# Kernel optimization log

Hardware: AMD Instinct MI355X
Metric: run time of the kernel (lower is better)

Reference implementation:

```python
import jax, jax.numpy as jnp
import numpy as np

LEAKY_SLOPE = 0.25
EPS_COS = 1e-8
EPS_NORM = 1e-12


def cosine_dist(x):
    # 1 - cosine similarity, matching cosine_distance_torch
    w = jnp.linalg.norm(x, axis=1, keepdims=True)  # [n,1]
    return 1.0 - (x @ x.T) / jnp.maximum(w * w.T, EPS_COS)


def gen_adj(x, edge_per_node):
    # gen_tr_adj_mat: threshold = (edge_per_node*n)-th smallest pairwise cosine distance,
    # zero diagonal, symmetrize via elementwise max, add I, L1 row-normalize.
    n = x.shape[0]
    dist = cosine_dist(x)  # [n,n]
    k = edge_per_node * n
    param = jax.lax.stop_gradient(jnp.partition(dist.ravel(), k)[k])
    eye = jnp.eye(n, dtype=x.dtype)
    g = (dist <= param).astype(x.dtype) * (1.0 - eye)
    adj = (1.0 - dist) * g
    adj_t = adj.T
    take_t = (adj_t > adj).astype(x.dtype)
    adj = adj + adj_t * take_t - adj * take_t  # elementwise max-symmetrize
    adj = adj + eye
    row_norm = jnp.maximum(jnp.sum(jnp.abs(adj), axis=1, keepdims=True), EPS_NORM)
    return adj / row_norm


def gcn_layer(x, adj, w, b):
    # dense mm -> (sparse) adj mm -> bias -> leaky_relu
    return jax.nn.leaky_relu(adj @ (x @ w) + b, LEAKY_SLOPE)


def setup_inputs() -> dict:
    key = jax.random.key(0)
    ks = jax.random.split(key, 8)
    n, d = 4000, 1000
    h = [400, 400, 200]
    x = jax.random.normal(ks[0], (n, d), jnp.float32)

    def xavier(k, fi, fo):
        std = (2.0 / (fi + fo)) ** 0.5
        return std * jax.random.normal(k, (fi, fo), jnp.float32)

    w1 = xavier(ks[1], d, h[0])
    w2 = xavier(ks[2], h[0], h[1])
    w3 = xavier(ks[3], h[1], h[2])
    b1 = jnp.zeros((h[0],), jnp.float32)
    b2 = jnp.zeros((h[1],), jnp.float32)
    b3 = jnp.zeros((h[2],), jnp.float32)
    adj_parameter = 10
    adj = gen_adj(x, adj_parameter)  # initial train adjacency, as in the pipeline
    return dict(adj_parameter=adj_parameter, x=x, adj=adj,
                w1=w1, b1=b1, w2=w2, b2=b2, w3=w3, b3=b3)


def reference(adj_parameter, x, adj, w1, b1, w2, b2, w3, b3):
    # eval mode: F.dropout(training=False) is identity
    x = gcn_layer(x, adj, w1, b1)
    adj = gen_adj(x, adj_parameter)
    x = gcn_layer(x, adj, w2, b2)
    adj = gen_adj(x, adj_parameter)
    x = gcn_layer(x, adj, w3, b3)
    return x
```

## Files before the change

### kernel.cpp

```cpp
#include <hip/hip_runtime.h>
#include <math.h>

#define NN 4000
#define KC 384
#define LEAKY 0.25f
#define HBLK 1000
#define NPART1 2016


template<int EPI>
__device__ inline float epi_apply(float v, int r, int c,
                                  const float* __restrict__ bias,
                                  const float* __restrict__ wn)
{
    if (EPI == 1) {
        float s = __fadd_rn(v, bias[c]);
        return (s >= 0.f) ? s : __fmul_rn(LEAKY, s);
    }
    if (EPI == 2) {
        float den = fmaxf(__fmul_rn(wn[r], wn[c]), 1e-8f);
        return __fsub_rn(1.0f, __fdiv_rn(v, den));
    }
    return v;
}

template<int XF>
__device__ float xf(float v)
{
    if (XF == 0) return __fmul_rn(v, v);
    return fabsf(v);
}

template<int XF>
__device__ float np_pairwise(const float* a, int n)
{
    if (n < 8) {
        float r = 0.f;
        for (int i = 0; i < n; ++i) r = __fadd_rn(r, xf<XF>(a[i]));
        return r;
    }
    if (n <= 128) {
        float r[8];
#pragma unroll
        for (int j = 0; j < 8; ++j) r[j] = xf<XF>(a[j]);
        int i = 8;
        const int lim = n - (n & 7);
        for (; i < lim; i += 8)
#pragma unroll
            for (int j = 0; j < 8; ++j) r[j] = __fadd_rn(r[j], xf<XF>(a[i + j]));
        float res = __fadd_rn(__fadd_rn(__fadd_rn(r[0], r[1]), __fadd_rn(r[2], r[3])),
                              __fadd_rn(__fadd_rn(r[4], r[5]), __fadd_rn(r[6], r[7])));
        for (; i < n; ++i) res = __fadd_rn(res, xf<XF>(a[i]));
        return res;
    }
    int n2 = (n / 2) & ~7;
    return __fadd_rn(np_pairwise<XF>(a, n2), np_pairwise<XF>(a + n2, n - n2));
}

__global__ __launch_bounds__(256, 4)
void gemm_tri64_k(const float* __restrict__ A, float* __restrict__ C,
                  unsigned* __restrict__ partial, int n, int K,
                  const float* __restrict__ wn)
{
    __shared__ float As[16][68];
    __shared__ float Bs[16][68];
    __shared__ unsigned lh[2048];
    const int tid = threadIdx.x;
    const int tx = tid & 15, ty = tid >> 4;
    const int sub = tid & 7;
    const int nt = (n + 63) >> 6;
    int bi = 0, rem = blockIdx.x;
    while (rem >= nt - bi) { rem -= nt - bi; ++bi; }
    const int bm = bi * 64, bn = (bi + rem) * 64;
    const bool diag = (rem == 0);

    for (int i = tid; i < 2048; i += 256) lh[i] = 0;

    float blk[4][4] = {};
    float acc[4][4];
    bool first = true;

    for (int kb = 0; kb < K; kb += KC) {
        const int kend = (kb + KC < K) ? kb + KC : K;
        for (int k0 = kb; k0 < kend; k0 += 16) {
            {
                int row = tid >> 2, q = tid & 3;
                int gr = bm + row, gk = k0 + q * 4;
                float4 v = make_float4(0.f, 0.f, 0.f, 0.f);
                if (gr < n) {
                    if (gk + 3 < kend) {
                        v = *(const float4*)(A + (size_t)gr * K + gk);
                    } else {
                        float* vp = (float*)&v;
#pragma unroll
                        for (int e = 0; e < 4; ++e)
                            if (gk + e < kend) vp[e] = A[(size_t)gr * K + gk + e];
                    }
                }
                float* vp = (float*)&v;
#pragma unroll
                for (int e = 0; e < 4; ++e) As[q * 4 + e][row] = vp[e];
            }
            {
                int row = tid >> 2, q = tid & 3;
                int gc = bn + row, gk = k0 + q * 4;
                float4 v = make_float4(0.f, 0.f, 0.f, 0.f);
                if (gc < n) {
                    if (gk + 3 < kend) {
                        v = *(const float4*)(A + (size_t)gc * K + gk);
                    } else {
                        float* vp = (float*)&v;
#pragma unroll
                        for (int e = 0; e < 4; ++e)
                            if (gk + e < kend) vp[e] = A[(size_t)gc * K + gk + e];
                    }
                }
                float* vp = (float*)&v;
#pragma unroll
                for (int e = 0; e < 4; ++e) Bs[q * 4 + e][row] = vp[e];
            }
            __syncthreads();
#pragma unroll
            for (int kk = 0; kk < 16; ++kk) {
                float a[4], b[4];
                *(float4*)&a[0] = *(const float4*)&As[kk][ty * 4];
                *(float4*)&b[0] = *(const float4*)&Bs[kk][tx * 4];
#pragma unroll
                for (int i = 0; i < 4; ++i)
#pragma unroll
                    for (int j = 0; j < 4; ++j)
                        blk[i][j] = fmaf(a[i], b[j], blk[i][j]);
            }
            __syncthreads();
        }
        if (first) {
#pragma unroll
            for (int i = 0; i < 4; ++i)
#pragma unroll
                for (int j = 0; j < 4; ++j) { acc[i][j] = blk[i][j]; blk[i][j] = 0.f; }
            first = false;
        } else {
#pragma unroll
            for (int i = 0; i < 4; ++i)
#pragma unroll
                for (int j = 0; j < 4; ++j) {
                    acc[i][j] = __fadd_rn(acc[i][j], blk[i][j]);
                    blk[i][j] = 0.f;
                }
        }
    }

#pragma unroll
    for (int i = 0; i < 4; ++i) {
        int r = bm + ty * 4 + i;
        if (r >= n) continue;
        float* Crow = C + (size_t)r * n;
        int c = bn + tx * 4;
        float v[4];
#pragma unroll
        for (int e = 0; e < 4; ++e)
            v[e] = epi_apply<2>(acc[i][e], r, c + e, nullptr, wn);
        if (c + 3 < n) {
            float4 s; s.x = v[0]; s.y = v[1]; s.z = v[2]; s.w = v[3];
            *(float4*)(Crow + c) = s;
        } else {
#pragma unroll
            for (int e = 0; e < 4; ++e)
                if (c + e < n) Crow[c + e] = v[e];
        }
#pragma unroll
        for (int e = 0; e < 4; ++e) {
            int cc = c + e;
            if (cc >= n) continue;
            unsigned w = 2u;
            if (diag) {
                if (cc < r) continue;
                if (cc == r) w = 1u;
            }
            unsigned u = __float_as_uint(v[e]);
            unsigned key = (u & 0x80000000u) ? ~u : (u | 0x80000000u);
            atomicAdd(&lh[(((key >> 24) & 0xFFu) << 3) | sub], w);
        }
    }
    __syncthreads();
    unsigned t = 0;
#pragma unroll
    for (int s = 0; s < 8; ++s) t += lh[(tid << 3) | s];
    partial[blockIdx.x * 256 + tid] = t;
}

template<int EPI>
__global__ __launch_bounds__(256, 4)
void gemm_s_k(const float* __restrict__ A, const float* __restrict__ B,
              float* __restrict__ C, int M, int N, int K,
              const float* __restrict__ bias)
{
    __shared__ float As[16][68];
    __shared__ float Bs[16][68];
    const int tid = threadIdx.x;
    const int tx = tid & 15, ty = tid >> 4;
    const int bm = blockIdx.y * 64, bn = blockIdx.x * 64;

    float blk[4][4] = {};
    float acc[4][4];
    bool first = true;

    for (int kb = 0; kb < K; kb += KC) {
        const int kend = (kb + KC < K) ? kb + KC : K;
        for (int k0 = kb; k0 < kend; k0 += 16) {
            {
                int row = tid >> 2, q = tid & 3;
                int gr = bm + row, gk = k0 + q * 4;
                float4 v = make_float4(0.f, 0.f, 0.f, 0.f);
                if (gr < M) {
                    if (gk + 3 < kend) {
                        v = *(const float4*)(A + (size_t)gr * K + gk);
                    } else {
                        float* vp = (float*)&v;
#pragma unroll
                        for (int e = 0; e < 4; ++e)
                            if (gk + e < kend) vp[e] = A[(size_t)gr * K + gk + e];
                    }
                }
                float* vp = (float*)&v;
#pragma unroll
                for (int e = 0; e < 4; ++e) As[q * 4 + e][row] = vp[e];
            }
            {
                int kk = tid >> 4, c = (tid & 15) * 4;
                int gk = k0 + kk, gc = bn + c;
                float4 v = make_float4(0.f, 0.f, 0.f, 0.f);
                if (gk < kend) {
                    if (gc + 3 < N) {
                        v = *(const float4*)(B + (size_t)gk * N + gc);
                    } else {
                        float* vp = (float*)&v;
#pragma unroll
                        for (int e = 0; e < 4; ++e)
                            if (gc + e < N) vp[e] = B[(size_t)gk * N + gc + e];
                    }
                }
                *(float4*)&Bs[kk][c] = v;
            }
            __syncthreads();
#pragma unroll
            for (int kk = 0; kk < 16; ++kk) {
                float a[4], b[4];
                *(float4*)&a[0] = *(const float4*)&As[kk][ty * 4];
                *(float4*)&b[0] = *(const float4*)&Bs[kk][tx * 4];
#pragma unroll
                for (int i = 0; i < 4; ++i)
#pragma unroll
                    for (int j = 0; j < 4; ++j)
                        blk[i][j] = fmaf(a[i], b[j], blk[i][j]);
            }
            __syncthreads();
        }
        if (first) {
#pragma unroll
            for (int i = 0; i < 4; ++i)
#pragma unroll
                for (int j = 0; j < 4; ++j) { acc[i][j] = blk[i][j]; blk[i][j] = 0.f; }
            first = false;
        } else {
#pragma unroll
            for (int i = 0; i < 4; ++i)
#pragma unroll
                for (int j = 0; j < 4; ++j) {
                    acc[i][j] = __fadd_rn(acc[i][j], blk[i][j]);
                    blk[i][j] = 0.f;
                }
        }
    }

#pragma unroll
    for (int i = 0; i < 4; ++i) {
        int r = bm + ty * 4 + i;
        if (r >= M) continue;
        float* Crow = C + (size_t)r * N;
        int c = bn + tx * 4;
        float v[4];
#pragma unroll
        for (int e = 0; e < 4; ++e)
            v[e] = epi_apply<EPI>(acc[i][e], r, c + e, bias, nullptr);
        if (c + 3 < N) {
            float4 s; s.x = v[0]; s.y = v[1]; s.z = v[2]; s.w = v[3];
            *(float4*)(Crow + c) = s;
        } else {
#pragma unroll
            for (int e = 0; e < 4; ++e)
                if (c + e < N) Crow[c + e] = v[e];
        }
    }
}

template<int EPI, bool TRANSB, bool FIRST, bool LAST>
__global__ __launch_bounds__(256, 4)
void gemm_pass_k(const float* __restrict__ A, const float* __restrict__ B,
                 float* __restrict__ C, int M, int N, int K, int kb, int kend,
                 const float* __restrict__ bias, const float* __restrict__ wn)
{
    __shared__ float As[16][132];
    __shared__ float Bs[16][132];
    const int tid = threadIdx.x;
    const int tx = tid & 15, ty = tid >> 4;
    const int bm = blockIdx.y * 128, bn = blockIdx.x * 128;

    float blk[8][8] = {};

    for (int k0 = kb; k0 < kend; k0 += 16) {
#pragma unroll
        for (int it = 0; it < 2; ++it) {
            int idx = tid + it * 256;
            int row = idx >> 2, q = idx & 3;
            int gr = bm + row, gk = k0 + q * 4;
            float4 v = make_float4(0.f, 0.f, 0.f, 0.f);
            if (gr < M) {
                if (gk + 3 < kend) {
                    v = *(const float4*)(A + (size_t)gr * K + gk);
                } else {
                    float* vp = (float*)&v;
#pragma unroll
                    for (int e = 0; e < 4; ++e)
                        if (gk + e < kend) vp[e] = A[(size_t)gr * K + gk + e];
                }
            }
            float* vp = (float*)&v;
#pragma unroll
            for (int e = 0; e < 4; ++e) As[q * 4 + e][row] = vp[e];
        }
        if (!TRANSB) {
#pragma unroll
            for (int it = 0; it < 2; ++it) {
                int idx = tid + it * 256;
                int kk = idx >> 5, cq = idx & 31;
                int gk = k0 + kk, c = cq * 4, gc = bn + c;
                float4 v = make_float4(0.f, 0.f, 0.f, 0.f);
                if (gk < kend) {
                    if (gc + 3 < N) {
                        v = *(const float4*)(B + (size_t)gk * N + gc);
                    } else {
                        float* vp = (float*)&v;
#pragma unroll
                        for (int e = 0; e < 4; ++e)
                            if (gc + e < N) vp[e] = B[(size_t)gk * N + gc + e];
                    }
                }
                *(float4*)&Bs[kk][c] = v;
            }
        } else {
#pragma unroll
            for (int it = 0; it < 2; ++it) {
                int idx = tid + it * 256;
                int row = idx >> 2, q = idx & 3;
                int gc = bn + row, gk = k0 + q * 4;
                float4 v = make_float4(0.f, 0.f, 0.f, 0.f);
                if (gc < N) {
                    if (gk + 3 < kend) {
                        v = *(const float4*)(B + (size_t)gc * K + gk);
                    } else {
                        float* vp = (float*)&v;
#pragma unroll
                        for (int e = 0; e < 4; ++e)
                            if (gk + e < kend) vp[e] = B[(size_t)gc * K + gk + e];
                    }
                }
                float* vp = (float*)&v;
#pragma unroll
                for (int e = 0; e < 4; ++e) Bs[q * 4 + e][row] = vp[e];
            }
        }
        __syncthreads();
#pragma unroll
        for (int kk = 0; kk < 16; ++kk) {
            float a[8], b[8];
            *(float4*)&a[0] = *(const float4*)&As[kk][ty * 4];
            *(float4*)&a[4] = *(const float4*)&As[kk][ty * 4 + 64];
            *(float4*)&b[0] = *(const float4*)&Bs[kk][tx * 4];
            *(float4*)&b[4] = *(const float4*)&Bs[kk][tx * 4 + 64];
#pragma unroll
            for (int i = 0; i < 8; ++i)
#pragma unroll
                for (int j = 0; j < 8; ++j)
                    blk[i][j] = fmaf(a[i], b[j], blk[i][j]);
        }
        __syncthreads();
    }

#pragma unroll
    for (int i = 0; i < 8; ++i) {
        int r = bm + ty * 4 + (i & 3) + (i >> 2) * 64;
        if (r >= M) continue;
        float* Crow = C + (size_t)r * N;
#pragma unroll
        for (int h = 0; h < 2; ++h) {
            int c = bn + tx * 4 + h * 64;
            float v[4];
#pragma unroll
            for (int e = 0; e < 4; ++e) v[e] = blk[i][h * 4 + e];
            if (c + 3 < N) {
                if (!FIRST) {
                    float4 o = *(const float4*)(Crow + c);
                    v[0] = __fadd_rn(o.x, v[0]); v[1] = __fadd_rn(o.y, v[1]);
                    v[2] = __fadd_rn(o.z, v[2]); v[3] = __fadd_rn(o.w, v[3]);
                }
                if (LAST) {
#pragma unroll
                    for (int e = 0; e < 4; ++e)
                        v[e] = epi_apply<EPI>(v[e], r, c + e, bias, wn);
                }
                float4 s; s.x = v[0]; s.y = v[1]; s.z = v[2]; s.w = v[3];
                *(float4*)(Crow + c) = s;
            } else {
#pragma unroll
                for (int e = 0; e < 4; ++e) {
                    if (c + e >= N) continue;
                    float vv = v[e];
                    if (!FIRST) vv = __fadd_rn(Crow[c + e], vv);
                    if (LAST) vv = epi_apply<EPI>(vv, r, c + e, bias, wn);
                    Crow[c + e] = vv;
                }
            }
        }
    }
}

__global__ __launch_bounds__(256)
void rownorm2_k(const float* __restrict__ X, float* __restrict__ wn)
{
    __shared__ float buf[400];
    __shared__ float leaf[4];
    const int row = blockIdx.x;
    const float* Xr = X + (size_t)row * 400;
    for (int i = threadIdx.x; i < 100; i += 256)
        *(float4*)&buf[i * 4] = *(const float4*)(Xr + i * 4);
    __syncthreads();
    if (threadIdx.x < 4) {
        const int off = (threadIdx.x >> 1) * 200 + ((threadIdx.x & 1) ? 96 : 0);
        const int len = (threadIdx.x & 1) ? 104 : 96;
        leaf[threadIdx.x] = np_pairwise<0>(buf + off, len);
    }
    __syncthreads();
    if (threadIdx.x == 0) {
        float s = __fadd_rn(__fadd_rn(leaf[0], leaf[1]),
                            __fadd_rn(leaf[2], leaf[3]));
        wn[row] = __fsqrt_rn(s);
    }
}

__global__ __launch_bounds__(256)
void rowabs2_k(const float* __restrict__ A, float* __restrict__ rs)
{
    __shared__ float buf[4000];
    __shared__ float leaf[8];
    const int row = blockIdx.x;
    const float* Ar = A + (size_t)row * 4000;
    for (int i = threadIdx.x; i < 1000; i += 256)
        *(float4*)&buf[i * 4] = *(const float4*)(Ar + i * 4);
    __syncthreads();
    if (threadIdx.x < 8) {
        const int off = (threadIdx.x >> 1) * 1000 + ((threadIdx.x & 1) ? 496 : 0);
        const int len = (threadIdx.x & 1) ? 504 : 496;
        leaf[threadIdx.x] = np_pairwise<1>(buf + off, len);
    }
    __syncthreads();
    if (threadIdx.x == 0) {
        float s = __fadd_rn(
            __fadd_rn(__fadd_rn(leaf[0], leaf[1]), __fadd_rn(leaf[2], leaf[3])),
            __fadd_rn(__fadd_rn(leaf[4], leaf[5]), __fadd_rn(leaf[6], leaf[7])));
        rs[row] = fmaxf(s, 1e-12f);
    }
}

__global__ void init_k(unsigned* __restrict__ state, const void* __restrict__ epn,
                       int* __restrict__ cnt)
{
    const int t = blockIdx.x * 256 + threadIdx.x;
    if (t < NN) cnt[t] = 0;
    if (t == 0) {
        int k = ((const int*)epn)[0];
        if (k <= 0 || k > 4000) {
            float f = ((const float*)epn)[0];
            if (f > 0.f && f <= 4000.f) k = (int)f;
            else {
                long long ll = ((const long long*)epn)[0];
                if (ll > 0 && ll <= 4000) k = (int)ll;
                else {
                    double dd = ((const double*)epn)[0];
                    k = (dd > 0.0 && dd <= 4000.0) ? (int)dd : 10;
                }
            }
        }
        state[0] = 0u;
        state[1] = (unsigned)(k * NN);
    }
}

__global__ __launch_bounds__(256)
void hist_tri_k(const float* __restrict__ dist, unsigned* __restrict__ partial,
                const unsigned* __restrict__ state, int shift, int n)
{
    __shared__ unsigned lh[2048];
    for (int i = threadIdx.x; i < 2048; i += 256) lh[i] = 0;
    __syncthreads();
    const unsigned prefix = state[0];
    const int sub = threadIdx.x & 7;
    const int npair = (n + 1) / 2;
    for (int p = blockIdx.x; p < npair; p += HBLK) {
#pragma unroll
        for (int half = 0; half < 2; ++half) {
            const int i = half ? (n - 1 - p) : p;
            if (half && i == p) break;
            const float* row = dist + (size_t)i * n;
            for (int j = i + threadIdx.x; j < n; j += 256) {
                unsigned u = __float_as_uint(row[j]);
                unsigned key = (u & 0x80000000u) ? ~u : (u | 0x80000000u);
                bool ok = ((key >> (shift + 8)) == prefix);
                if (ok) atomicAdd(&lh[((((key >> shift) & 0xFFu)) << 3) | sub],
                                  (j == i) ? 1u : 2u);
            }
        }
    }
    __syncthreads();
    unsigned t = 0;
#pragma unroll
    for (int s = 0; s < 8; ++s) t += lh[(threadIdx.x << 3) | s];
    partial[blockIdx.x * 256 + threadIdx.x] = t;
}

__global__ __launch_bounds__(256)
void reduce_k(const unsigned* __restrict__ partial, int nparts,
              unsigned* __restrict__ hist256)
{
    const int bin = blockIdx.x;
    const int tid = threadIdx.x;
    unsigned s = 0;
    for (int i = tid; i < nparts; i += 256)
        s += partial[(size_t)i * 256 + bin];
    __shared__ unsigned sh[256];
    sh[tid] = s;
    __syncthreads();
    for (int off = 128; off > 0; off >>= 1) {
        if (tid < off) sh[tid] += sh[tid + off];
        __syncthreads();
    }
    if (tid == 0) hist256[bin] = sh[0];
}

__global__ __launch_bounds__(256)
void scan256_k(const unsigned* __restrict__ hist256, unsigned* __restrict__ state,
               int shift, float* __restrict__ param)
{
    const int tid = threadIdx.x;
    unsigned h = hist256[tid];
    __shared__ unsigned sh[256];
    sh[tid] = h;
    __syncthreads();
    for (int off = 1; off < 256; off <<= 1) {
        unsigned v = (tid >= off) ? sh[tid - off] : 0;
        __syncthreads();
        sh[tid] += v;
        __syncthreads();
    }
    const unsigned incl = sh[tid], excl = incl - h;
    const unsigned krem = state[1];
    if (krem >= excl && krem < incl) {
        unsigned np = (state[0] << 8) | (unsigned)tid;
        state[0] = np;
        state[1] = krem - excl;
        if (shift == 0) {
            unsigned u = (np & 0x80000000u) ? (np ^ 0x80000000u) : ~np;
            *param = __uint_as_float(u);
        }
    }
}

__device__ inline float thr_f(float d, int i, int j, float p)
{
    float a = (d <= p && i != j) ? __fsub_rn(1.0f, d) : 0.0f;
    return (i == j) ? 1.0f : a;
}

__global__ __launch_bounds__(256)
void symthresh_mirror_k(float* __restrict__ adj, const float* __restrict__ param,
                        int* __restrict__ cnt, int n)
{
    __shared__ float TB[64][65];
    const float p = *param;
    const int nt = (n + 63) >> 6;
    int bi = 0, rem = blockIdx.x;
    while (rem >= nt - bi) { rem -= nt - bi; ++bi; }
    const int bj = bi + rem;
    const int tid = threadIdx.x;
    const int lane = tid & 63;
    const int r0i = bi * 64, r0j = bj * 64;

#pragma unroll
    for (int it = 0; it < 16; ++it) {
        int idx = tid + it * 256;
        int q = idx >> 6, c = idx & 63;
        int gr = r0i + q, gc = r0j + c;
        bool inb = (gr < n && gc < n);
        float a = 0.f;
        if (inb) {
            a = thr_f(adj[(size_t)gr * n + gc], gr, gc, p);
            adj[(size_t)gr * n + gc] = a;
            TB[q][c] = a;
        }
        unsigned long long m = __ballot(inb && a != 0.0f);
        if (lane == 0 && gr < n) atomicAdd(&cnt[gr], (int)__popcll(m));
    }
    __syncthreads();
    if (bi != bj) {
#pragma unroll
        for (int it = 0; it < 16; ++it) {
            int idx = tid + it * 256;
            int q = idx >> 6, c = idx & 63;
            int gr = r0j + q, gc = r0i + c;
            bool inb = (gr < n && gc < n);
            float a = 0.f;
            if (inb) {
                a = TB[c][q];
                adj[(size_t)gr * n + gc] = a;
            }
            unsigned long long m = __ballot(inb && a != 0.0f);
            if (lane == 0 && gr < n) atomicAdd(&cnt[gr], (int)__popcll(m));
        }
    }
}

__global__ __launch_bounds__(256)
void norm_k(float* __restrict__ adj, const float* __restrict__ rs, int n)
{
    const int i = blockIdx.y;
    const int j = blockIdx.x * 256 + threadIdx.x;
    if (j >= n) return;
    const size_t idx = (size_t)i * n + j;
    adj[idx] = __fdiv_rn(adj[idx], rs[i]);
}

__global__ __launch_bounds__(256)
void count_k(const float* __restrict__ A, int* __restrict__ cnt, int n)
{
    const int gw = (blockIdx.x * blockDim.x + threadIdx.x) >> 6;
    if (gw >= n) return;
    const int lane = threadIdx.x & 63;
    int c = 0;
    for (int k0 = 0; k0 < n; k0 += 64) {
        int k = k0 + lane;
        bool nz = (k < n) && (A[(size_t)gw * n + k] != 0.0f);
        unsigned long long m = __ballot(nz);
        c += (int)__popcll(m);
    }
    if (lane == 0) cnt[gw] = c;
}

__global__ __launch_bounds__(1024)
void scanrows_k(const int* __restrict__ cnt, int* __restrict__ roff)
{
    const int t = threadIdx.x;
    int vals[4];
    int s0 = 0;
#pragma unroll
    for (int e = 0; e < 4; ++e) {
        int r = t * 4 + e;
        vals[e] = (r < NN) ? cnt[r] : 0;
        s0 += vals[e];
    }
    __shared__ int sh[1024];
    sh[t] = s0;
    __syncthreads();
    for (int off = 1; off < 1024; off <<= 1) {
        int v = (t >= off) ? sh[t - off] : 0;
        __syncthreads();
        sh[t] += v;
        __syncthreads();
    }
    int excl = sh[t] - s0;
#pragma unroll
    for (int e = 0; e < 4; ++e) {
        int r = t * 4 + e;
        if (r <= NN) roff[r] = excl;
        excl += vals[e];
    }
    if (t == 1023) roff[NN] = sh[1023];
}

template<bool DIV>
__global__ __launch_bounds__(256)
void fill_k(const float* __restrict__ A, const int* __restrict__ roff,
            const float* __restrict__ rs, int* __restrict__ ridx,
            float* __restrict__ rval, int n)
{
    const int gw = (blockIdx.x * blockDim.x + threadIdx.x) >> 6;
    if (gw >= n) return;
    const int lane = threadIdx.x & 63;
    const float r = DIV ? rs[gw] : 1.0f;
    int base = roff[gw];
    const unsigned long long ltmask = (lane == 63) ? ~0ULL >> 1
                                                   : ((1ULL << lane) - 1);
    for (int k0 = 0; k0 < n; k0 += 64) {
        int k = k0 + lane;
        float v = (k < n) ? A[(size_t)gw * n + k] : 0.f;
        bool nz = (v != 0.0f);
        unsigned long long m = __ballot(nz);
        if (nz) {
            int pos = base + (int)__popcll(m & ltmask);
            ridx[pos] = k;
            rval[pos] = DIV ? __fdiv_rn(v, r) : v;
        }
        base += (int)__popcll(m);
    }
}

template<bool WN>
__global__ __launch_bounds__(256)
void spmm_k(const int* __restrict__ roff, const int* __restrict__ ridx,
            const float* __restrict__ rval, const float* __restrict__ T,
            const float* __restrict__ bias, float* __restrict__ H, int ncols,
            float* __restrict__ wn)
{
    __shared__ int ks[128];
    __shared__ float vs[128];
    __shared__ float buf[512];
    __shared__ float leaf[4];
    const int r = blockIdx.x;
    const int tid = threadIdx.x;
    const int c0 = tid, c1 = tid + 256;
    const bool ok0 = c0 < ncols, ok1 = c1 < ncols;
    float acc0 = 0.f, blk0 = 0.f, acc1 = 0.f, blk1 = 0.f;
    int nb = KC;
    const int s = roff[r], e = roff[r + 1];
    for (int base = s; base < e; base += 128) {
        const int m = (e - base < 128) ? (e - base) : 128;
        __syncthreads();
        if (tid < m) { ks[tid] = ridx[base + tid]; vs[tid] = rval[base + tid]; }
        __syncthreads();
        for (int t = 0; t < m; ++t) {
            const int k = ks[t];
            const float v = vs[t];
            while (k >= nb) {
                acc0 = __fadd_rn(acc0, blk0); blk0 = 0.f;
                acc1 = __fadd_rn(acc1, blk1); blk1 = 0.f;
                nb += KC;
            }
            const float* Tr = T + (size_t)k * ncols;
            if (ok0) blk0 = fmaf(v, Tr[c0], blk0);
            if (ok1) blk1 = fmaf(v, Tr[c1], blk1);
        }
    }
    acc0 = __fadd_rn(acc0, blk0);
    acc1 = __fadd_rn(acc1, blk1);
    float h0 = 0.f, h1 = 0.f;
    if (ok0) {
        float s0 = __fadd_rn(acc0, bias[c0]);
        h0 = (s0 >= 0.f) ? s0 : __fmul_rn(LEAKY, s0);
        H[(size_t)r * ncols + c0] = h0;
    }
    if (ok1) {
        float s1 = __fadd_rn(acc1, bias[c1]);
        h1 = (s1 >= 0.f) ? s1 : __fmul_rn(LEAKY, s1);
        H[(size_t)r * ncols + c1] = h1;
    }
    if (WN) {
        if (ok0) buf[c0] = h0;
        if (ok1) buf[c1] = h1;
        __syncthreads();
        if (tid < 4) {
            const int off = (tid >> 1) * 200 + ((tid & 1) ? 96 : 0);
            const int len = (tid & 1) ? 104 : 96;
            leaf[tid] = np_pairwise<0>(buf + off, len);
        }
        __syncthreads();
        if (tid == 0) {
            float s2 = __fadd_rn(__fadd_rn(leaf[0], leaf[1]),
                                 __fadd_rn(leaf[2], leaf[3]));
            wn[r] = __fsqrt_rn(s2);
        }
    }
}

template<int EPI, bool TRANSB>
static void run_gemm(const float* A, const float* B, float* C,
                     int M, int N, int K, const float* bias, const float* wn,
                     hipStream_t stream)
{
    const int nb = (K + KC - 1) / KC;
    const dim3 grid((N + 127) / 128, (M + 127) / 128);
    for (int p = 0; p < nb; ++p) {
        const int kb = p * KC;
        const int kend = (kb + KC < K) ? kb + KC : K;
        const bool first = (p == 0), last = (p == nb - 1);
        if (first && last)
            gemm_pass_k<EPI, TRANSB, true, true><<<grid, 256, 0, stream>>>(
                A, B, C, M, N, K, kb, kend, bias, wn);
        else if (first)
            gemm_pass_k<EPI, TRANSB, true, false><<<grid, 256, 0, stream>>>(
                A, B, C, M, N, K, kb, kend, bias, wn);
        else if (last)
            gemm_pass_k<EPI, TRANSB, false, true><<<grid, 256, 0, stream>>>(
                A, B, C, M, N, K, kb, kend, bias, wn);
        else
            gemm_pass_k<EPI, TRANSB, false, false><<<grid, 256, 0, stream>>>(
                A, B, C, M, N, K, kb, kend, bias, wn);
    }
}

extern "C" void kernel_launch(void* const* d_in, const int* in_sizes, int n_in,
                              void* d_out, int out_size, void* d_ws, size_t ws_size,
                              hipStream_t stream)
{
    const void*  epn  = d_in[0];
    const float* x    = (const float*)d_in[1];
    const float* adj0 = (const float*)d_in[2];
    const float* w1   = (const float*)d_in[3];
    const float* b1   = (const float*)d_in[4];
    const float* w2   = (const float*)d_in[5];
    const float* b2   = (const float*)d_in[6];
    const float* w3   = (const float*)d_in[7];
    const float* b3   = (const float*)d_in[8];
    float* out = (float*)d_out;

    char* ws = (char*)d_ws;
    float*    dist    = (float*)   ws;
    float*    Tbuf    = (float*)  (ws + 64000000);
    float*    H1      = (float*)  (ws + 70400000);
    float*    H2      = (float*)  (ws + 76800000);
    float*    wn      = (float*)  (ws + 83200000);
    float*    rs      = (float*)  (ws + 83216000);
    unsigned* state   = (unsigned*)(ws + 83232000);
    float*    param   = (float*)  (ws + 83232008);
    unsigned* hist256 = (unsigned*)(ws + 83232064);
    unsigned* partial = (unsigned*)(ws + 83233088);
    int*      cnt     = (int*)    (ws + 85297472);
    int*      roff    = (int*)    (ws + 85313472);
    int*      ridx    = (int*)    (ws + 85329480);
    float*    rval    = (float*)  (ws + 101329480);
    const bool use_csr = (ws_size >= 117329480ULL + 64);

    const int gsN = (NN + 63) / 64;
    const int nt64 = (NN + 63) / 64;
    const int nsym64 = nt64 * (nt64 + 1) / 2;

    auto genadj = [&](const float* H, bool have_wn) {
        if (!have_wn)
            rownorm2_k<<<NN, 256, 0, stream>>>(H, wn);
        gemm_tri64_k<<<nsym64, 256, 0, stream>>>(H, dist, partial, NN, 400, wn);
        init_k<<<16, 256, 0, stream>>>(state, epn, cnt);
        reduce_k<<<256, 256, 0, stream>>>(partial, NPART1, hist256);
        scan256_k<<<1, 256, 0, stream>>>(hist256, state, 24, param);
        for (int p = 1; p < 4; ++p) {
            const int shift = 24 - 8 * p;
            hist_tri_k<<<HBLK, 256, 0, stream>>>(dist, partial, state, shift, NN);
            reduce_k<<<256, 256, 0, stream>>>(partial, HBLK, hist256);
            scan256_k<<<1, 256, 0, stream>>>(hist256, state, shift, param);
        }
        symthresh_mirror_k<<<nsym64, 256, 0, stream>>>(dist, param, cnt, NN);
        rowabs2_k<<<NN, 256, 0, stream>>>(dist, rs);
    };

    auto aggregate_pre = [&](const float* Aadj, const float* Tm,
                             const float* bias, float* Hout, int ncols,
                             bool want_wn) {
        if (use_csr) {
            count_k<<<(NN + 3) / 4, 256, 0, stream>>>(Aadj, cnt, NN);
            scanrows_k<<<1, 1024, 0, stream>>>(cnt, roff);
            fill_k<false><<<(NN + 3) / 4, 256, 0, stream>>>(Aadj, roff, nullptr,
                                                            ridx, rval, NN);
            if (want_wn)
                spmm_k<true><<<NN, 256, 0, stream>>>(roff, ridx, rval, Tm, bias,
                                                     Hout, ncols, wn);
            else
                spmm_k<false><<<NN, 256, 0, stream>>>(roff, ridx, rval, Tm, bias,
                                                      Hout, ncols, nullptr);
        } else {
            run_gemm<1, false>(Aadj, Tm, Hout, NN, ncols, NN, bias,
                               nullptr, stream);
        }
    };

    auto aggregate_rs = [&](float* Aadj, const float* Tm,
                            const float* bias, float* Hout, int ncols,
                            bool want_wn) {
        if (use_csr) {
            scanrows_k<<<1, 1024, 0, stream>>>(cnt, roff);
            fill_k<true><<<(NN + 3) / 4, 256, 0, stream>>>(Aadj, roff, rs,
                                                           ridx, rval, NN);
            if (want_wn)
                spmm_k<true><<<NN, 256, 0, stream>>>(roff, ridx, rval, Tm, bias,
                                                     Hout, ncols, wn);
            else
                spmm_k<false><<<NN, 256, 0, stream>>>(roff, ridx, rval, Tm, bias,
                                                      Hout, ncols, nullptr);
        } else {
            norm_k<<<dim3((NN + 255) / 256, NN), 256, 0, stream>>>(Aadj, rs, NN);
            run_gemm<1, false>(Aadj, Tm, Hout, NN, ncols, NN, bias,
                               nullptr, stream);
        }
    };

    gemm_s_k<0><<<dim3((400 + 63) / 64, gsN), 256, 0, stream>>>(
        x, w1, Tbuf, NN, 400, 1000, nullptr);
    aggregate_pre(adj0, Tbuf, b1, H1, 400, use_csr);

    genadj(H1, use_csr);
    gemm_s_k<0><<<dim3((400 + 63) / 64, gsN), 256, 0, stream>>>(
        H1, w2, Tbuf, NN, 400, 400, nullptr);
    aggregate_rs(dist, Tbuf, b2, H2, 400, use_csr);

    genadj(H2, use_csr);
    gemm_s_k<0><<<dim3((200 + 63) / 64, gsN), 256, 0, stream>>>(
        H2, w3, Tbuf, NN, 200, 400, nullptr);
    aggregate_rs(dist, Tbuf, b3, out, 200, false);
}
```

Before: 881.8 us.

## Split first GEMM over K into panels, raise occupancy, alias LDS histogram

Turns the first x@w1 GEMM into a split-K launch that writes three K-panel partial products, followed by a separate combine kernel that sums them. This gives more blocks than the 7x63 grid for better CU fill. The triangular distance GEMM now reuses the tile shared memory for its histogram, cutting LDS use, and launch bounds on several kernels go from 4 to 8 blocks per CU. The costs are extra panel traffic plus a combine pass, and possible register pressure from the tighter launch bounds.

```diff
diff --git a/kernel.cpp b/kernel.cpp
--- a/kernel.cpp
+++ b/kernel.cpp
@@ -57,14 +57,15 @@
     return __fadd_rn(np_pairwise<XF>(a, n2), np_pairwise<XF>(a + n2, n - n2));
 }
 
-__global__ __launch_bounds__(256, 4)
+__global__ __launch_bounds__(256, 8)
 void gemm_tri64_k(const float* __restrict__ A, float* __restrict__ C,
                   unsigned* __restrict__ partial, int n, int K,
                   const float* __restrict__ wn)
 {
-    __shared__ float As[16][68];
-    __shared__ float Bs[16][68];
-    __shared__ unsigned lh[2048];
+    __shared__ float smem[2176];
+    float (*As)[68] = reinterpret_cast<float(*)[68]>(smem);
+    float (*Bs)[68] = reinterpret_cast<float(*)[68]>(smem + 1088);
+    unsigned* lh = reinterpret_cast<unsigned*>(smem);
     const int tid = threadIdx.x;
     const int tx = tid & 15, ty = tid >> 4;
     const int sub = tid & 7;
@@ -73,8 +74,6 @@
     while (rem >= nt - bi) { rem -= nt - bi; ++bi; }
     const int bm = bi * 64, bn = (bi + rem) * 64;
     const bool diag = (rem == 0);
-
-    for (int i = tid; i < 2048; i += 256) lh[i] = 0;
 
     float blk[4][4] = {};
     float acc[4][4];
@@ -150,6 +149,9 @@
         }
     }
 
+    for (int i = tid; i < 2048; i += 256) lh[i] = 0;
+    __syncthreads();
+
 #pragma unroll
     for (int i = 0; i < 4; ++i) {
         int r = bm + ty * 4 + i;
@@ -190,7 +192,7 @@
 }
 
 template<int EPI>
-__global__ __launch_bounds__(256, 4)
+__global__ __launch_bounds__(256, 8)
 void gemm_s_k(const float* __restrict__ A, const float* __restrict__ B,
               float* __restrict__ C, int M, int N, int K,
               const float* __restrict__ bias)
@@ -294,25 +296,24 @@
     }
 }
 
-template<int EPI, bool TRANSB, bool FIRST, bool LAST>
-__global__ __launch_bounds__(256, 4)
-void gemm_pass_k(const float* __restrict__ A, const float* __restrict__ B,
-                 float* __restrict__ C, int M, int N, int K, int kb, int kend,
-                 const float* __restrict__ bias, const float* __restrict__ wn)
-{
-    __shared__ float As[16][132];
-    __shared__ float Bs[16][132];
+__global__ __launch_bounds__(256, 8)
+void gemm_panel_k(const float* __restrict__ A, const float* __restrict__ B,
+                  float* __restrict__ P, int M, int N, int K)
+{
+    __shared__ float As[16][68];
+    __shared__ float Bs[16][68];
     const int tid = threadIdx.x;
     const int tx = tid & 15, ty = tid >> 4;
-    const int bm = blockIdx.y * 128, bn = blockIdx.x * 128;
-
-    float blk[8][8] = {};
+    const int bm = blockIdx.y * 64, bn = blockIdx.x * 64;
+    const int kb = blockIdx.z * KC;
+    const int kend = (kb + KC < K) ? kb + KC : K;
+    float* Pp = P + (size_t)blockIdx.z * M * N;
+
+    float blk[4][4] = {};
 
     for (int k0 = kb; k0 < kend; k0 += 16) {
-#pragma unroll
-        for (int it = 0; it < 2; ++it) {
-            int idx = tid + it * 256;
-            int row = idx >> 2, q = idx & 3;
+        {
+            int row = tid >> 2, q = tid & 3;
             int gr = bm + row, gk = k0 + q * 4;
             float4 v = make_float4(0.f, 0.f, 0.f, 0.f);
             if (gr < M) {
@@ -329,99 +330,71 @@
 #pragma unroll
             for (int e = 0; e < 4; ++e) As[q * 4 + e][row] = vp[e];
         }
-        if (!TRANSB) {
-#pragma unroll
-            for (int it = 0; it < 2; ++it) {
-                int idx = tid + it * 256;
-                int kk = idx >> 5, cq = idx & 31;
-                int gk = k0 + kk, c = cq * 4, gc = bn + c;
-                float4 v = make_float4(0.f, 0.f, 0.f, 0.f);
-                if (gk < kend) {
-                    if (gc + 3 < N) {
-                        v = *(const float4*)(B + (size_t)gk * N + gc);
-                    } else {
-                        float* vp = (float*)&v;
-#pragma unroll
-                        for (int e = 0; e < 4; ++e)
-                            if (gc + e < N) vp[e] = B[(size_t)gk * N + gc + e];
-                    }
-                }
-                *(float4*)&Bs[kk][c] = v;
-            }
+        {
+            int kk = tid >> 4, c = (tid & 15) * 4;
+            int gk = k0 + kk, gc = bn + c;
+            float4 v = make_float4(0.f, 0.f, 0.f, 0.f);
+            if (gk < kend) {
+                if (gc + 3 < N) {
+                    v = *(const float4*)(B + (size_t)gk * N + gc);
+                } else {
+                    float* vp = (float*)&v;
+#pragma unroll
+                    for (int e = 0; e < 4; ++e)
+                        if (gc + e < N) vp[e] = B[(size_t)gk * N + gc + e];
+                }
+            }
+            *(float4*)&Bs[kk][c] = v;
+        }
+        __syncthreads();
+#pragma unroll
+        for (int kk = 0; kk < 16; ++kk) {
+            float a[4], b[4];
+            *(float4*)&a[0] = *(const float4*)&As[kk][ty * 4];
+            *(float4*)&b[0] = *(const float4*)&Bs[kk][tx * 4];
+#pragma unroll
+            for (int i = 0; i < 4; ++i)
+#pragma unroll
+                for (int j = 0; j < 4; ++j)
+                    blk[i][j] = fmaf(a[i], b[j], blk[i][j]);
+        }
+        __syncthreads();
+    }
+
+#pragma unroll
+    for (int i = 0; i < 4; ++i) {
+        int r = bm + ty * 4 + i;
+        if (r >= M) continue;
+        float* Prow = Pp + (size_t)r * N;
+        int c = bn + tx * 4;
+        if (c + 3 < N) {
+            float4 s; s.x = blk[i][0]; s.y = blk[i][1];
+            s.z = blk[i][2]; s.w = blk[i][3];
+            *(float4*)(Prow + c) = s;
         } else {
 #pragma unroll
-            for (int it = 0; it < 2; ++it) {
-                int idx = tid + it * 256;
-                int row = idx >> 2, q = idx & 3;
-                int gc = bn + row, gk = k0 + q * 4;
-                float4 v = make_float4(0.f, 0.f, 0.f, 0.f);
-                if (gc < N) {
-                    if (gk + 3 < kend) {
-                        v = *(const float4*)(B + (size_t)gc * K + gk);
-                    } else {
-                        float* vp = (float*)&v;
-#pragma unroll
-                        for (int e = 0; e < 4; ++e)
-                            if (gk + e < kend) vp[e] = B[(size_t)gc * K + gk + e];
-                    }
-                }
-                float* vp = (float*)&v;
-#pragma unroll
-                for (int e = 0; e < 4; ++e) Bs[q * 4 + e][row] = vp[e];
-            }
-        }
-        __syncthreads();
-#pragma unroll
-        for (int kk = 0; kk < 16; ++kk) {
-            float a[8], b[8];
-            *(float4*)&a[0] = *(const float4*)&As[kk][ty * 4];
-            *(float4*)&a[4] = *(const float4*)&As[kk][ty * 4 + 64];
-            *(float4*)&b[0] = *(const float4*)&Bs[kk][tx * 4];
-            *(float4*)&b[4] = *(const float4*)&Bs[kk][tx * 4 + 64];
-#pragma unroll
-            for (int i = 0; i < 8; ++i)
-#pragma unroll
-                for (int j = 0; j < 8; ++j)
-                    blk[i][j] = fmaf(a[i], b[j], blk[i][j]);
-        }
-        __syncthreads();
-    }
-
-#pragma unroll
-    for (int i = 0; i < 8; ++i) {
-        int r = bm + ty * 4 + (i & 3) + (i >> 2) * 64;
-        if (r >= M) continue;
-        float* Crow = C + (size_t)r * N;
-#pragma unroll
-        for (int h = 0; h < 2; ++h) {
-            int c = bn + tx * 4 + h * 64;
-            float v[4];
-#pragma unroll
-            for (int e = 0; e < 4; ++e) v[e] = blk[i][h * 4 + e];
-            if (c + 3 < N) {
-                if (!FIRST) {
-                    float4 o = *(const float4*)(Crow + c);
-                    v[0] = __fadd_rn(o.x, v[0]); v[1] = __fadd_rn(o.y, v[1]);
-                    v[2] = __fadd_rn(o.z, v[2]); v[3] = __fadd_rn(o.w, v[3]);
-                }
-                if (LAST) {
-#pragma unroll
-                    for (int e = 0; e < 4; ++e)
-                        v[e] = epi_apply<EPI>(v[e], r, c + e, bias, wn);
-                }
-                float4 s; s.x = v[0]; s.y = v[1]; s.z = v[2]; s.w = v[3];
-                *(float4*)(Crow + c) = s;
-            } else {
-#pragma unroll
-                for (int e = 0; e < 4; ++e) {
-                    if (c + e >= N) continue;
-                    float vv = v[e];
-                    if (!FIRST) vv = __fadd_rn(Crow[c + e], vv);
-                    if (LAST) vv = epi_apply<EPI>(vv, r, c + e, bias, wn);
-                    Crow[c + e] = vv;
-                }
-            }
-        }
+            for (int e = 0; e < 4; ++e)
+                if (c + e < N) Prow[c + e] = blk[i][e];
+        }
+    }
+}
+
+__global__ __launch_bounds__(256)
+void combine3_k(const float* __restrict__ P, float* __restrict__ C, size_t nelem)
+{
+    const size_t i4 = (size_t)(blockIdx.x * 256 + threadIdx.x);
+    const size_t stride = (size_t)gridDim.x * 256;
+    const size_t n4 = nelem / 4;
+    for (size_t i = i4; i < n4; i += stride) {
+        float4 a = *(const float4*)(P + i * 4);
+        float4 b = *(const float4*)(P + nelem + i * 4);
+        float4 c = *(const float4*)(P + 2 * nelem + i * 4);
+        float4 o;
+        o.x = __fadd_rn(__fadd_rn(a.x, b.x), c.x);
+        o.y = __fadd_rn(__fadd_rn(a.y, b.y), c.y);
+        o.z = __fadd_rn(__fadd_rn(a.z, b.z), c.z);
+        o.w = __fadd_rn(__fadd_rn(a.w, b.w), c.w);
+        *(float4*)(C + i * 4) = o;
     }
 }
 
@@ -776,6 +749,137 @@
             float s2 = __fadd_rn(__fadd_rn(leaf[0], leaf[1]),
                                  __fadd_rn(leaf[2], leaf[3]));
             wn[r] = __fsqrt_rn(s2);
+        }
+    }
+}
+
+template<int EPI, bool TRANSB, bool FIRST, bool LAST>
+__global__ __launch_bounds__(256, 4)
+void gemm_pass_k(const float* __restrict__ A, const float* __restrict__ B,
+                 float* __restrict__ C, int M, int N, int K, int kb, int kend,
+                 const float* __restrict__ bias, const float* __restrict__ wn)
+{
+    __shared__ float As[16][132];
+    __shared__ float Bs[16][132];
+    const int tid = threadIdx.x;
+    const int tx = tid & 15, ty = tid >> 4;
+    const int bm = blockIdx.y * 128, bn = blockIdx.x * 128;
+
+    float blk[8][8] = {};
+
+    for (int k0 = kb; k0 < kend; k0 += 16) {
+#pragma unroll
+        for (int it = 0; it < 2; ++it) {
+            int idx = tid + it * 256;
+            int row = idx >> 2, q = idx & 3;
+            int gr = bm + row, gk = k0 + q * 4;
+            float4 v = make_float4(0.f, 0.f, 0.f, 0.f);
+            if (gr < M) {
+                if (gk + 3 < kend) {
+                    v = *(const float4*)(A + (size_t)gr * K + gk);
+                } else {
+                    float* vp = (float*)&v;
+#pragma unroll
+                    for (int e = 0; e < 4; ++e)
+                        if (gk + e < kend) vp[e] = A[(size_t)gr * K + gk + e];
+                }
+            }
+            float* vp = (float*)&v;
+#pragma unroll
+            for (int e = 0; e < 4; ++e) As[q * 4 + e][row] = vp[e];
+        }
+        if (!TRANSB) {
+#pragma unroll
+            for (int it = 0; it < 2; ++it) {
+                int idx = tid + it * 256;
+                int kk = idx >> 5, cq = idx & 31;
+                int gk = k0 + kk, c = cq * 4, gc = bn + c;
+                float4 v = make_float4(0.f, 0.f, 0.f, 0.f);
+                if (gk < kend) {
+                    if (gc + 3 < N) {
+                        v = *(const float4*)(B + (size_t)gk * N + gc);
+                    } else {
+                        float* vp = (float*)&v;
+#pragma unroll
+                        for (int e = 0; e < 4; ++e)
+                            if (gc + e < N) vp[e] = B[(size_t)gk * N + gc + e];
+                    }
+                }
+                *(float4*)&Bs[kk][c] = v;
+            }
+        } else {
+#pragma unroll
+            for (int it = 0; it < 2; ++it) {
+                int idx = tid + it * 256;
+                int row = idx >> 2, q = idx & 3;
+                int gc = bn + row, gk = k0 + q * 4;
+                float4 v = make_float4(0.f, 0.f, 0.f, 0.f);
+                if (gc < N) {
+                    if (gk + 3 < kend) {
+                        v = *(const float4*)(B + (size_t)gc * K + gk);
+                    } else {
+                        float* vp = (float*)&v;
+#pragma unroll
+                        for (int e = 0; e < 4; ++e)
+                            if (gk + e < kend) vp[e] = B[(size_t)gc * K + gk + e];
+                    }
+                }
+                float* vp = (float*)&v;
+#pragma unroll
+                for (int e = 0; e < 4; ++e) Bs[q * 4 + e][row] = vp[e];
+            }
+        }
+        __syncthreads();
+#pragma unroll
+        for (int kk = 0; kk < 16; ++kk) {
+            float a[8], b[8];
+            *(float4*)&a[0] = *(const float4*)&As[kk][ty * 4];
+            *(float4*)&a[4] = *(const float4*)&As[kk][ty * 4 + 64];
+            *(float4*)&b[0] = *(const float4*)&Bs[kk][tx * 4];
+            *(float4*)&b[4] = *(const float4*)&Bs[kk][tx * 4 + 64];
+#pragma unroll
+            for (int i = 0; i < 8; ++i)
+#pragma unroll
+                for (int j = 0; j < 8; ++j)
+                    blk[i][j] = fmaf(a[i], b[j], blk[i][j]);
+        }
+        __syncthreads();
+    }
+
+#pragma unroll
+    for (int i = 0; i < 8; ++i) {
+        int r = bm + ty * 4 + (i & 3) + (i >> 2) * 64;
+        if (r >= M) continue;
+        float* Crow = C + (size_t)r * N;
+#pragma unroll
+        for (int h = 0; h < 2; ++h) {
+            int c = bn + tx * 4 + h * 64;
+            float v[4];
+#pragma unroll
+            for (int e = 0; e < 4; ++e) v[e] = blk[i][h * 4 + e];
+            if (c + 3 < N) {
+                if (!FIRST) {
+                    float4 o = *(const float4*)(Crow + c);
+                    v[0] = __fadd_rn(o.x, v[0]); v[1] = __fadd_rn(o.y, v[1]);
+                    v[2] = __fadd_rn(o.z, v[2]); v[3] = __fadd_rn(o.w, v[3]);
+                }
+                if (LAST) {
+#pragma unroll
+                    for (int e = 0; e < 4; ++e)
+                        v[e] = epi_apply<EPI>(v[e], r, c + e, bias, wn);
+                }
+                float4 s; s.x = v[0]; s.y = v[1]; s.z = v[2]; s.w = v[3];
+                *(float4*)(Crow + c) = s;
+            } else {
+#pragma unroll
+                for (int e = 0; e < 4; ++e) {
+                    if (c + e >= N) continue;
+                    float vv = v[e];
+                    if (!FIRST) vv = __fadd_rn(Crow[c + e], vv);
+                    if (LAST) vv = epi_apply<EPI>(vv, r, c + e, bias, wn);
+                    Crow[c + e] = vv;
+                }
+            }
         }
     }
 }
@@ -836,6 +940,7 @@
     int*      roff    = (int*)    (ws + 85313472);
     int*      ridx    = (int*)    (ws + 85329480);
     float*    rval    = (float*)  (ws + 101329480);
+    float*    panels  = (float*)  (ws + 85329480);
     const bool use_csr = (ws_size >= 117329480ULL + 64);
 
     const int gsN = (NN + 63) / 64;
@@ -899,8 +1004,14 @@
         }
     };
 
-    gemm_s_k<0><<<dim3((400 + 63) / 64, gsN), 256, 0, stream>>>(
-        x, w1, Tbuf, NN, 400, 1000, nullptr);
+    if (use_csr) {
+        gemm_panel_k<<<dim3((400 + 63) / 64, gsN, 3), 256, 0, stream>>>(
+            x, w1, panels, NN, 400, 1000);
+        combine3_k<<<1024, 256, 0, stream>>>(panels, Tbuf, (size_t)NN * 400);
+    } else {
+        gemm_s_k<0><<<dim3((400 + 63) / 64, gsN), 256, 0, stream>>>(
+            x, w1, Tbuf, NN, 400, 1000, nullptr);
+    }
     aggregate_pre(adj0, Tbuf, b1, H1, 400, use_csr);
 
     genadj(H1, use_csr);
```

Result: slower. 925.9 us, median of 2 (+5.0%).
